# Kernel tuning notes

Hardware: AMD Instinct MI355X
Metric: run time of the kernel (lower is better)

The kernel has to match this reference:

```python
import jax, jax.numpy as jnp
import numpy as np

B, C, H, W = 8, 64, 256, 256  # H must equal W for the second matmul


def setup_inputs() -> dict:
    key = jax.random.key(0)
    kq, kk, kv = jax.random.split(key, 3)
    Q = jax.random.normal(kq, (B, C, H, W), dtype=jnp.float32)
    K = jax.random.normal(kk, (B, C, H, W), dtype=jnp.float32)
    V = jax.random.normal(kv, (B, C, H, W), dtype=jnp.float32)
    di = jnp.ones((1,), dtype=jnp.float32)  # learned scalar scale
    return {"Q": Q, "K": K, "V": V, "di": di}


def reference(Q, K, V, di):
    # similarity[b,c,i,k] = sum_w Q[b,c,i,w] * K[b,c,k,w], scaled by di
    sim = jnp.einsum('bciw,bckw->bcik', Q, K) * di[0]
    attn = jax.nn.softmax(sim, axis=-1)  # [B,C,H,H]
    # residual = attn @ V^T -> [B,C,H,H]; output is residual^T:
    # out[b,c,i,j] = sum_k attn[b,c,j,k] * V[b,c,i,k]
    out = jnp.einsum('bcjk,bcik->bcij', attn, V)
    return out
```

## Files before the change

kernel.cpp:

```cpp
#include <hip/hip_runtime.h>
#include <hip/hip_bf16.h>


typedef __attribute__((ext_vector_type(8))) _Float16 f16x8;
typedef __attribute__((ext_vector_type(4))) float f32x4;
typedef __attribute__((ext_vector_type(16))) float f32x16;

#define BARRIER() asm volatile("s_waitcnt lgkmcnt(0)\n\ts_barrier" ::: "memory")

__device__ __forceinline__ f32x4 mfma16h(f16x8 a, f16x8 b, f32x4 c) {
  return __builtin_amdgcn_mfma_f32_16x16x32_f16(a, b, c, 0, 0, 0);
}
__device__ __forceinline__ f32x16 mfma32h(f16x8 a, f16x8 b, f32x16 c) {
  return __builtin_amdgcn_mfma_f32_32x32x16_f16(a, b, c, 0, 0, 0);
}
__device__ __forceinline__ f16x8 cvt8(f32x4 a, f32x4 b) {
  f16x8 r;
  r[0] = (_Float16)a[0]; r[1] = (_Float16)a[1];
  r[2] = (_Float16)a[2]; r[3] = (_Float16)a[3];
  r[4] = (_Float16)b[0]; r[5] = (_Float16)b[1];
  r[6] = (_Float16)b[2]; r[7] = (_Float16)b[3];
  return r;
}
__device__ __forceinline__ int swzA(int row, int byteCol) {
  return row * 512 + (byteCol ^ ((row & 15) << 4));
}
__device__ __forceinline__ int swzV(int row, int byteCol) {
  return row * 256 + (byteCol ^ ((row & 15) << 4));
}

__global__ __launch_bounds__(1024, 4) void attn_fused11(
    const float* __restrict__ Q, const float* __restrict__ K,
    const float* __restrict__ V, const float* __restrict__ di,
    float* __restrict__ out) {
  __shared__ short Kbuf[2][16 * 256];
  __shared__ short Abuf[256 * 256];
  short* Vlds = &Kbuf[0][0];

  const int t = threadIdx.x;
  const int lane = t & 63;
  const int wv = t >> 6;
  const int l15 = lane & 15;
  const int l4 = (lane >> 4) & 3;
  const int l31 = lane & 31;
  const int h5 = lane >> 5;

  const int bc = blockIdx.x;

  const float dival = di[0];
  const size_t base = (size_t)bc << 16;
  const float* Qs = Q + base;
  const float* Ks = K + base;
  const float* Vs = V + base;
  float* Os = out + base;

  const int sr = t >> 6;
  const int scf = (t & 63) << 2;

  f32x4 kpA, kpB;
  {
    const float* p = Ks + sr * 256 + scf;
    kpA = *(const f32x4*)p;
    kpB = *(const f32x4*)(p + 4096);
  }
  f16x8 qh[8];
  {
    const float* qrow = Qs + (size_t)(16 * wv + l15) * 256 + 8 * l4;
#pragma unroll
    for (int s = 0; s < 8; ++s)
      qh[s] = cvt8(*(const f32x4*)(qrow + 32 * s),
                   *(const f32x4*)(qrow + 32 * s + 4));
  }

  f32x4 acc[16];
#pragma unroll
  for (int i = 0; i < 16; ++i) acc[i] = (f32x4){0.f, 0.f, 0.f, 0.f};

#pragma unroll
  for (int ch = 0; ch < 16; ++ch) {
    short* kb = Kbuf[ch & 1];
    {
      _Float16 h4[4];
      f32x4 src = ((ch & 1) == 0) ? kpA : kpB;
      h4[0] = (_Float16)src[0];
      h4[1] = (_Float16)src[1];
      h4[2] = (_Float16)src[2];
      h4[3] = (_Float16)src[3];
      *(unsigned long long*)((char*)kb + swzA(sr, scf * 2)) =
          *(unsigned long long*)h4;
    }
    BARRIER();
    if (ch < 14) {
      const float* p = Ks + (ch + 2) * 4096 + sr * 256 + scf;
      if ((ch & 1) == 0)
        kpA = *(const f32x4*)p;
      else
        kpB = *(const f32x4*)p;
    }
    __builtin_amdgcn_s_setprio(1);
    f32x4 a = acc[ch];
#pragma unroll
    for (int s = 0; s < 8; ++s) {
      f16x8 bh = *(const f16x8*)((const char*)kb + swzA(l15, 64 * s + 16 * l4));
      a = mfma16h(qh[s], bh, a);
    }
    acc[ch] = a;
    __builtin_amdgcn_s_setprio(0);
  }

  const int vr = t >> 4;
  const int vcf = (t & 15) * 8;
  f32x4 vpA[2], vpB[2];
  {
    const float* p = Vs + (size_t)vr * 256 + vcf;
    vpA[0] = *(const f32x4*)p;
    vpA[1] = *(const f32x4*)(p + 4);
    const float* q = p + 128;
    vpB[0] = *(const f32x4*)q;
    vpB[1] = *(const f32x4*)(q + 4);
  }

  float mx[4] = {-1e30f, -1e30f, -1e30f, -1e30f};
#pragma unroll
  for (int idx = 0; idx < 16; ++idx)
#pragma unroll
    for (int r = 0; r < 4; ++r) {
      acc[idx][r] *= dival;
      mx[r] = fmaxf(mx[r], acc[idx][r]);
    }
#pragma unroll
  for (int o = 1; o <= 8; o <<= 1)
#pragma unroll
    for (int r = 0; r < 4; ++r) mx[r] = fmaxf(mx[r], __shfl_xor(mx[r], o));
  float sm[4] = {0.f, 0.f, 0.f, 0.f};
#pragma unroll
  for (int idx = 0; idx < 16; ++idx)
#pragma unroll
    for (int r = 0; r < 4; ++r) {
      acc[idx][r] = __expf(acc[idx][r] - mx[r]);
      sm[r] += acc[idx][r];
    }
#pragma unroll
  for (int o = 1; o <= 8; o <<= 1)
#pragma unroll
    for (int r = 0; r < 4; ++r) sm[r] += __shfl_xor(sm[r], o);
#pragma unroll
  for (int r = 0; r < 4; ++r) sm[r] = 1.0f / sm[r];
#pragma unroll
  for (int idx = 0; idx < 16; ++idx)
#pragma unroll
    for (int r = 0; r < 4; ++r) {
      const int row = 16 * wv + 4 * l4 + r;
      *(_Float16*)((char*)Abuf + swzA(row, 2 * (16 * idx + l15))) =
          (_Float16)(acc[idx][r] * sm[r]);
    }
  BARRIER();

  const int ig = wv & 1;
  const int jg = wv >> 1;
  f32x16 o = {};
#pragma unroll
  for (int cc = 0; cc < 8; ++cc) {
    const int kh = cc & 1;
    if ((cc & 1) == 0) {
      *(f16x8*)((char*)Vlds + swzV(vr, 2 * vcf)) = cvt8(vpA[0], vpA[1]);
      BARRIER();
      if (cc < 6) {
        const float* p = Vs + (size_t)(64 * ((cc + 2) >> 1) + vr) * 256 + vcf;
        vpA[0] = *(const f32x4*)p;
        vpA[1] = *(const f32x4*)(p + 4);
      }
    } else {
      *(f16x8*)((char*)Vlds + swzV(vr, 2 * vcf)) = cvt8(vpB[0], vpB[1]);
      BARRIER();
      if (cc < 6) {
        const float* p =
            Vs + (size_t)(64 * ((cc + 2) >> 1) + vr) * 256 + 128 + vcf;
        vpB[0] = *(const f32x4*)p;
        vpB[1] = *(const f32x4*)(p + 4);
      }
    }
    __builtin_amdgcn_s_setprio(1);
#pragma unroll
    for (int kk = 0; kk < 8; ++kk) {
      f16x8 vfrag = *(const f16x8*)((const char*)Vlds +
                                    swzV(32 * ig + l31, 32 * kk + 16 * h5));
      f16x8 pfrag =
          *(const f16x8*)((const char*)Abuf +
                          swzA(32 * jg + l31, 256 * kh + 32 * kk + 16 * h5));
      o = mfma32h(vfrag, pfrag, o);
    }
    __builtin_amdgcn_s_setprio(0);
    if (kh == 1) {
      const int rbase = 64 * (cc >> 1) + 32 * ig + 4 * h5;
      const int col = 32 * jg + l31;
#pragma unroll
      for (int reg = 0; reg < 16; ++reg) {
        const int rw = (reg & 3) + 8 * (reg >> 2);
        Os[(size_t)(rbase + rw) * 256 + col] = o[reg];
      }
      o = (f32x16){};
    }
    BARRIER();
  }
}

extern "C" void kernel_launch(void* const* d_in, const int* in_sizes, int n_in,
                              void* d_out, int out_size, void* d_ws,
                              size_t ws_size, hipStream_t stream) {
  const float* Q = (const float*)d_in[0];
  const float* K = (const float*)d_in[1];
  const float* V = (const float*)d_in[2];
  const float* di = (const float*)d_in[3];
  float* out = (float*)d_out;
  const int BC = in_sizes[0] / (256 * 256);
  hipLaunchKernelGGL(attn_fused11, dim3(BC), dim3(1024), 0, stream, Q, K, V,
                     di, out);
}
```

Baseline: 106.8 us.

## Double K staging chunk size and double-buffer V tiles to cut barriers

```diff
diff --git a/kernel.cpp b/kernel.cpp
--- a/kernel.cpp
+++ b/kernel.cpp
@@ -29,13 +29,14 @@
   return row * 256 + (byteCol ^ ((row & 15) << 4));
 }
 
-__global__ __launch_bounds__(1024, 4) void attn_fused11(
+__global__ __launch_bounds__(1024, 4) void attn_fused13(
     const float* __restrict__ Q, const float* __restrict__ K,
     const float* __restrict__ V, const float* __restrict__ di,
     float* __restrict__ out) {
-  __shared__ short Kbuf[2][16 * 256];
+  __shared__ short Kbuf[2][32 * 256];
   __shared__ short Abuf[256 * 256];
-  short* Vlds = &Kbuf[0][0];
+  short* Vlds0 = &Kbuf[0][0];
+  short* Vlds1 = &Kbuf[1][0];
 
   const int t = threadIdx.x;
   const int lane = t & 63;
@@ -54,14 +55,16 @@
   const float* Vs = V + base;
   float* Os = out + base;
 
-  const int sr = t >> 6;
-  const int scf = (t & 63) << 2;
-
-  f32x4 kpA, kpB;
+  const int sr = t >> 5;
+  const int scf = (t & 31) << 3;
+
+  f32x4 kpA0, kpA1, kpB0, kpB1;
   {
     const float* p = Ks + sr * 256 + scf;
-    kpA = *(const f32x4*)p;
-    kpB = *(const f32x4*)(p + 4096);
+    kpA0 = *(const f32x4*)p;
+    kpA1 = *(const f32x4*)(p + 4);
+    kpB0 = *(const f32x4*)(p + 8192);
+    kpB1 = *(const f32x4*)(p + 8192 + 4);
   }
   f16x8 qh[8];
   {
@@ -77,34 +80,37 @@
   for (int i = 0; i < 16; ++i) acc[i] = (f32x4){0.f, 0.f, 0.f, 0.f};
 
 #pragma unroll
-  for (int ch = 0; ch < 16; ++ch) {
+  for (int ch = 0; ch < 8; ++ch) {
     short* kb = Kbuf[ch & 1];
-    {
-      _Float16 h4[4];
-      f32x4 src = ((ch & 1) == 0) ? kpA : kpB;
-      h4[0] = (_Float16)src[0];
-      h4[1] = (_Float16)src[1];
-      h4[2] = (_Float16)src[2];
-      h4[3] = (_Float16)src[3];
-      *(unsigned long long*)((char*)kb + swzA(sr, scf * 2)) =
-          *(unsigned long long*)h4;
+    if ((ch & 1) == 0) {
+      *(f16x8*)((char*)kb + swzA(sr, scf * 2)) = cvt8(kpA0, kpA1);
+    } else {
+      *(f16x8*)((char*)kb + swzA(sr, scf * 2)) = cvt8(kpB0, kpB1);
     }
     BARRIER();
-    if (ch < 14) {
-      const float* p = Ks + (ch + 2) * 4096 + sr * 256 + scf;
-      if ((ch & 1) == 0)
-        kpA = *(const f32x4*)p;
-      else
-        kpB = *(const f32x4*)p;
+    if (ch < 6) {
+      const float* p = Ks + (ch + 2) * 8192 + sr * 256 + scf;
+      if ((ch & 1) == 0) {
+        kpA0 = *(const f32x4*)p;
+        kpA1 = *(const f32x4*)(p + 4);
+      } else {
+        kpB0 = *(const f32x4*)p;
+        kpB1 = *(const f32x4*)(p + 4);
+      }
     }
     __builtin_amdgcn_s_setprio(1);
-    f32x4 a = acc[ch];
-#pragma unroll
-    for (int s = 0; s < 8; ++s) {
-      f16x8 bh = *(const f16x8*)((const char*)kb + swzA(l15, 64 * s + 16 * l4));
-      a = mfma16h(qh[s], bh, a);
-    }
-    acc[ch] = a;
+#pragma unroll
+    for (int kf = 0; kf < 2; ++kf) {
+      const int kr = 16 * kf + l15;
+      f32x4 a = acc[2 * ch + kf];
+#pragma unroll
+      for (int s = 0; s < 8; ++s) {
+        f16x8 bh =
+            *(const f16x8*)((const char*)kb + swzA(kr, 64 * s + 16 * l4));
+        a = mfma16h(qh[s], bh, a);
+      }
+      acc[2 * ch + kf] = a;
+    }
     __builtin_amdgcn_s_setprio(0);
   }
 
@@ -162,20 +168,20 @@
 #pragma unroll
   for (int cc = 0; cc < 8; ++cc) {
     const int kh = cc & 1;
+    short* vb = (cc & 1) ? Vlds1 : Vlds0;
     if ((cc & 1) == 0) {
-      *(f16x8*)((char*)Vlds + swzV(vr, 2 * vcf)) = cvt8(vpA[0], vpA[1]);
-      BARRIER();
-      if (cc < 6) {
-        const float* p = Vs + (size_t)(64 * ((cc + 2) >> 1) + vr) * 256 + vcf;
+      *(f16x8*)((char*)vb + swzV(vr, 2 * vcf)) = cvt8(vpA[0], vpA[1]);
+    } else {
+      *(f16x8*)((char*)vb + swzV(vr, 2 * vcf)) = cvt8(vpB[0], vpB[1]);
+    }
+    BARRIER();
+    if (cc < 6) {
+      const float* p = Vs + (size_t)(64 * ((cc + 2) >> 1) + vr) * 256 +
+                       ((cc & 1) ? 128 : 0) + vcf;
+      if ((cc & 1) == 0) {
         vpA[0] = *(const f32x4*)p;
         vpA[1] = *(const f32x4*)(p + 4);
-      }
-    } else {
-      *(f16x8*)((char*)Vlds + swzV(vr, 2 * vcf)) = cvt8(vpB[0], vpB[1]);
-      BARRIER();
-      if (cc < 6) {
-        const float* p =
-            Vs + (size_t)(64 * ((cc + 2) >> 1) + vr) * 256 + 128 + vcf;
+      } else {
         vpB[0] = *(const f32x4*)p;
         vpB[1] = *(const f32x4*)(p + 4);
       }
@@ -183,7 +189,7 @@
     __builtin_amdgcn_s_setprio(1);
 #pragma unroll
     for (int kk = 0; kk < 8; ++kk) {
-      f16x8 vfrag = *(const f16x8*)((const char*)Vlds +
+      f16x8 vfrag = *(const f16x8*)((const char*)vb +
                                     swzV(32 * ig + l31, 32 * kk + 16 * h5));
       f16x8 pfrag =
           *(const f16x8*)((const char*)Abuf +
@@ -201,7 +207,6 @@
       }
       o = (f32x16){};
     }
-    BARRIER();
   }
 }
 
@@ -214,6 +219,6 @@
   const float* di = (const float*)d_in[3];
   float* out = (float*)d_out;
   const int BC = in_sizes[0] / (256 * 256);
-  hipLaunchKernelGGL(attn_fused11, dim3(BC), dim3(1024), 0, stream, Q, K, V,
+  hipLaunchKernelGGL(attn_fused13, dim3(BC), dim3(1024), 0, stream, Q, K, V,
                      di, out);
 }
```

Result: no change. 105.5 us (-1.2%).
